# Performance work log

Measured on AMD Instinct MI355X. Metric: run time of the kernel, lower is better.

Reference implementation:

```python
import jax, jax.numpy as jnp
import numpy as np


def _ccl(x, w, b):
    # FFT-domain circular conv: rfft2 -> complex multiply + sum over c_in -> irfft2 + bias
    H, W = x.shape[-2], x.shape[-1]
    xf = jnp.fft.rfft2(x)                 # [B, Ci, H, Wf] complex
    wf = jnp.fft.rfft2(w, s=(H, W))       # [Co, Ci, H, Wf] complex
    hf = jnp.einsum('bihw,oihw->bohw', xf, wf)
    return jnp.fft.irfft2(hf, s=(H, W)) + b[:, None, None]


def _maxpool(x, ph, pw):
    B, C, H, W = x.shape
    return x.reshape(B, C, H // ph, ph, W // pw, pw).max(axis=(3, 5))


def _upsample_zero(x, sh, sw):
    B, C, H, W = x.shape
    y = jnp.zeros((B, C, H * sh, W * sw), dtype=x.dtype)
    return y.at[:, :, ::sh, ::sw].set(x)


def setup_inputs() -> dict:
    key = jax.random.key(0)
    ks = jax.random.split(key, 11)
    inp = {"x": jax.random.normal(ks[0], (16, 2, 64, 256), dtype=jnp.float32)}
    specs = [  # (c_out, c_in, kh, kw)
        (50, 1, 3, 7), (50, 50, 3, 7), (50, 50, 3, 5), (50, 50, 3, 7), (1, 50, 3, 7)]
    for i, (co, ci, kh, kw) in enumerate(specs):
        K = float(np.sqrt(1.0 / (ci * kh * kw)))
        inp[f"w{i+1}"] = (2 * jax.random.uniform(ks[2 * i + 1], (co, ci, kh, kw), dtype=jnp.float32) - 1) * K
        inp[f"b{i+1}"] = (2 * jax.random.uniform(ks[2 * i + 2], (co,), dtype=jnp.float32) - 1) * K
    return inp


def reference(x, w1, b1, w2, b2, w3, b3, w4, b4, w5, b5):
    H, W = x.shape[-2], x.shape[-1]
    h = x.reshape(-1, 1, H, W)                       # [2B, 1, 64, 256]
    h = jax.nn.relu(_maxpool(_ccl(h, w1, b1), 2, 4))  # [2B, 50, 32, 64]
    h = jax.nn.relu(_maxpool(_ccl(h, w2, b2), 2, 4))  # [2B, 50, 16, 16]
    h = h.reshape(-1, 2, h.shape[-3], h.shape[-2], h.shape[-1])
    h = h[:, 0] + h[:, 1].mean(axis=(-1, -2))[..., None, None]  # [B, 50, 16, 16]
    h = jax.nn.relu(_ccl(_upsample_zero(h, 2, 4), w3, b3))       # [B, 50, 32, 64]
    h = jax.nn.relu(_ccl(_upsample_zero(h, 2, 4), w4, b4))       # [B, 50, 64, 256]
    h = jax.nn.sigmoid(_ccl(h, w5, b5))                          # [B, 1, 64, 256]
    return h.squeeze(1)
```

## Files before the change

### kernel.cpp

```cpp
#include <hip/hip_runtime.h>
#include <math.h>

__global__ __launch_bounds__(256) void k1(const float* __restrict__ x,
                                          const float* __restrict__ w1,
                                          const float* __restrict__ b1,
                                          float* __restrict__ a1,
                                          const float* __restrict__ w2,
                                          const float* __restrict__ w3,
                                          const float* __restrict__ w4,
                                          float* __restrict__ w2t,
                                          float* __restrict__ w3t,
                                          float* __restrict__ w4t) {
  int b = blockIdx.z;
  int pr0 = blockIdx.x * 4;
  int co0 = blockIdx.y * 10;
  int ty = threadIdx.x >> 6;
  int pc = threadIdx.x & 63;
  int pr = pr0 + ty;
  const float* xb = x + b * (64 * 256);
  float xw[4][12];
#pragma unroll
  for (int r = 0; r < 4; ++r) {
    int row = (2 * pr - 2 + r) & 63;
    const float* rb = xb + row * 256;
#pragma unroll
    for (int v = 0; v < 3; ++v) {
      int col = (4 * pc - 8 + 4 * v) & 255;
      float4 t = *(const float4*)&rb[col];
      xw[r][4 * v + 0] = t.x; xw[r][4 * v + 1] = t.y;
      xw[r][4 * v + 2] = t.z; xw[r][4 * v + 3] = t.w;
    }
  }
#pragma unroll
  for (int cq = 0; cq < 10; ++cq) {
    int co = co0 + cq;
    const float* wp = w1 + co * 21;
    float m = -1e30f;
#pragma unroll
    for (int iy = 0; iy < 2; ++iy) {
#pragma unroll
      for (int jx = 0; jx < 4; ++jx) {
        float s = 0.f;
#pragma unroll
        for (int di = 0; di < 3; ++di)
#pragma unroll
          for (int dj = 0; dj < 7; ++dj)
            s = fmaf(xw[iy + 2 - di][jx + 8 - dj], wp[di * 7 + dj], s);
        m = fmaxf(m, s);
      }
    }
    float v = fmaxf(m + b1[co], 0.f);
    a1[((b * 50 + co) * 32 + pr) * 64 + pc] = v;
  }
  if (blockIdx.y == 0) {
    int base = (blockIdx.z * 8 + blockIdx.x) * 256 + threadIdx.x;
    for (int i = base; i < 90000; i += 65536) {
      if (i < 52500) {
        int co = i % 50, r = i / 50;
        w2t[i] = w2[co * 1050 + r];
        w4t[i] = w4[co * 1050 + r];
      } else {
        int j2 = i - 52500;
        int co = j2 % 50, r = j2 / 50;
        w3t[j2] = w3[co * 750 + r];
      }
    }
  }
}

__global__ __launch_bounds__(256) void k2(const float* __restrict__ a1,
                                          const float* __restrict__ w2t,
                                          const float* __restrict__ b2,
                                          float* __restrict__ a2) {
  __shared__ __align__(16) float sm[3840];
  int b = blockIdx.z;
  int r0 = blockIdx.x * 4;
  int co0 = blockIdx.y * 10;
  int y = threadIdx.x >> 6;
  int xcol = threadIdx.x & 63;
  const float* p[7];
#pragma unroll
  for (int dj = 0; dj < 7; ++dj) p[dj] = sm + y * 64 + ((xcol - dj) & 63);
  float acc[10];
#pragma unroll
  for (int co = 0; co < 10; ++co) acc[co] = b2[co0 + co];
  const float* ain = a1 + b * (50 * 2048);
  for (int cci = 0; cci < 5; ++cci) {
    __syncthreads();
    for (int e = threadIdx.x; e < 960; e += 256) {
      int ci = e / 96;
      int rem = e - ci * 96;
      int rr = rem >> 4;
      int c4 = rem & 15;
      int row = (r0 - 2 + rr) & 31;
      *(float4*)&sm[(ci * 6 + rr) * 64 + c4 * 4] =
          *(const float4*)&ain[(cci * 10 + ci) * 2048 + row * 64 + c4 * 4];
    }
    __syncthreads();
    const float* q0 = p[0]; const float* q1 = p[1]; const float* q2 = p[2];
    const float* q3 = p[3]; const float* q4 = p[4]; const float* q5 = p[5];
    const float* q6 = p[6];
    for (int ci = 0; ci < 10; ++ci) {
      const float* wci = w2t + (cci * 10 + ci) * 1050 + co0;
#pragma unroll
      for (int di = 0; di < 3; ++di) {
        const int ro = (2 - di) * 64;
        float xv0 = q0[ro], xv1 = q1[ro], xv2 = q2[ro], xv3 = q3[ro];
        float xv4 = q4[ro], xv5 = q5[ro], xv6 = q6[ro];
        const float* wr = wci + di * 7 * 50;
#pragma unroll
        for (int co = 0; co < 10; ++co) acc[co] = fmaf(xv0, wr[co], acc[co]);
#pragma unroll
        for (int co = 0; co < 10; ++co) acc[co] = fmaf(xv1, wr[50 + co], acc[co]);
#pragma unroll
        for (int co = 0; co < 10; ++co) acc[co] = fmaf(xv2, wr[100 + co], acc[co]);
#pragma unroll
        for (int co = 0; co < 10; ++co) acc[co] = fmaf(xv3, wr[150 + co], acc[co]);
#pragma unroll
        for (int co = 0; co < 10; ++co) acc[co] = fmaf(xv4, wr[200 + co], acc[co]);
#pragma unroll
        for (int co = 0; co < 10; ++co) acc[co] = fmaf(xv5, wr[250 + co], acc[co]);
#pragma unroll
        for (int co = 0; co < 10; ++co) acc[co] = fmaf(xv6, wr[300 + co], acc[co]);
      }
      q0 += 384; q1 += 384; q2 += 384; q3 += 384; q4 += 384; q5 += 384; q6 += 384;
    }
  }
  __syncthreads();
#pragma unroll
  for (int k = 0; k < 10; ++k)
    sm[k * 256 + y * 64 + xcol] = acc[k];
  __syncthreads();
  for (int w = threadIdx.x; w < 320; w += 256) {
    int cop = w / 32;
    int pr = (w >> 4) & 1;
    int pc = w & 15;
    float m = -1e30f;
#pragma unroll
    for (int yy = 0; yy < 2; ++yy)
#pragma unroll
      for (int xx = 0; xx < 4; ++xx)
        m = fmaxf(m, sm[cop * 256 + (pr * 2 + yy) * 64 + pc * 4 + xx]);
    m = fmaxf(m, 0.f);
    a2[((b * 50 + co0 + cop) * 16 + (r0 >> 1) + pr) * 16 + pc] = m;
  }
}

__global__ __launch_bounds__(512) void k3(const float* __restrict__ a2,
                                          const float* __restrict__ w3t,
                                          const float* __restrict__ b3,
                                          float* __restrict__ a3) {
  __shared__ float ts[4000];
  __shared__ float mean_s[64];
  __shared__ float part[200];
  int b = blockIdx.z;
  int r0 = blockIdx.x * 8;
  int co0 = blockIdx.y * 5;
  int tid = threadIdx.x;
  const float* aodd = a2 + (2 * b + 1) * (50 * 256);
  if (tid < 200) {
    int ci = tid >> 2, p = tid & 3;
    float s = 0.f;
    for (int k = 0; k < 64; ++k) s += aodd[ci * 256 + p * 64 + k];
    part[tid] = s;
  }
  __syncthreads();
  if (tid < 50)
    mean_s[tid] = (part[4 * tid] + part[4 * tid + 1] + part[4 * tid + 2] + part[4 * tid + 3]) * (1.f / 256.f);
  __syncthreads();
  const float* aev = a2 + (2 * b) * (50 * 256);
  for (int e = tid; e < 4000; e += 512) {
    int ci = e / 80;
    int rr = (e >> 4) % 5;
    int tc = e & 15;
    int trow = ((r0 >> 1) - 1 + rr) & 15;
    ts[e] = aev[ci * 256 + trow * 16 + tc] + mean_s[ci];
  }
  __syncthreads();
  int wv = __builtin_amdgcn_readfirstlane(tid >> 6);
  int lane = tid & 63;
  int p = wv >> 2;
  int m = wv & 3;
  int q = lane & 15;
  int yidx = lane >> 4;
  int i = r0 + 2 * yidx + p;
  int j = 4 * q + m;
  float acc[5];
#pragma unroll
  for (int co = 0; co < 5; ++co) acc[co] = b3[co0 + co];
  int ndi = (p == 0) ? 2 : 1;
  int ndj = (m == 0) ? 2 : 1;
  for (int aa = 0; aa < ndi; ++aa) {
    int di = (p == 0) ? (2 * aa) : 1;
    int rr = 1 + ((2 * yidx + p - di) >> 1);
    for (int e2 = 0; e2 < ndj; ++e2) {
      int dj = (m == 0) ? (4 * e2) : m;
      int tc = ((j - dj + 64) >> 2) & 15;
      for (int ci = 0; ci < 50; ++ci) {
        float xv = ts[ci * 80 + rr * 16 + tc];
        const float* wrow = w3t + (ci * 15 + di * 5 + dj) * 50 + co0;
#pragma unroll
        for (int co = 0; co < 5; ++co)
          acc[co] = fmaf(xv, wrow[co], acc[co]);
      }
    }
  }
  float* aout = a3 + b * (50 * 2048);
#pragma unroll
  for (int co = 0; co < 5; ++co)
    aout[(co0 + co) * 2048 + i * 64 + j] = fmaxf(acc[co], 0.f);
}

__global__ __launch_bounds__(512) void k4(const float* __restrict__ a3,
                                          const float* __restrict__ w4t,
                                          const float* __restrict__ b4,
                                          float* __restrict__ a4) {
  __shared__ __align__(16) float s4[9600];
  int b = blockIdx.z;
  int r0 = blockIdx.x * 4;
  int co0 = blockIdx.y * 10;
  int tid = threadIdx.x;
  const float* ain = a3 + b * (50 * 2048);
  int prb = (r0 >> 1) - 1;
  for (int e = tid; e < 2400; e += 512) {
    int ci = e / 48;
    int rem = e - ci * 48;
    int rr = rem >> 4;
    int c4 = rem & 15;
    int row = (prb + rr) & 31;
    *(float4*)&s4[(ci * 3 + rr) * 64 + c4 * 4] =
        *(const float4*)&ain[ci * 2048 + row * 64 + c4 * 4];
  }
  __syncthreads();
  int wv = __builtin_amdgcn_readfirstlane(tid >> 6);
  int lane = tid & 63;
  int rowsel = wv >> 2;
  int m = wv & 3;
  int j = 4 * lane + m;
  float acc[2][10];
#pragma unroll
  for (int co = 0; co < 10; ++co) {
    float bc = b4[co0 + co];
    acc[0][co] = bc; acc[1][co] = bc;
  }
  int ndi = (rowsel == 0) ? 2 : 1;
  int ndj = (m < 3) ? 2 : 1;
  for (int aa = 0; aa < ndi; ++aa) {
    int di = (rowsel == 0) ? (2 * aa) : 1;
    int rrb = 1 + ((rowsel - di) >> 1);
    for (int e2 = 0; e2 < ndj; ++e2) {
      int dj = m + 4 * e2;
      int tc = ((j - dj) >> 2) & 63;
      for (int ci = 0; ci < 50; ++ci) {
        float xv0 = s4[ci * 192 + rrb * 64 + tc];
        float xv1 = s4[ci * 192 + (rrb + 1) * 64 + tc];
        const float* wrow = w4t + (ci * 21 + di * 7 + dj) * 50 + co0;
#pragma unroll
        for (int co = 0; co < 10; ++co) {
          float w = wrow[co];
          acc[0][co] = fmaf(xv0, w, acc[0][co]);
          acc[1][co] = fmaf(xv1, w, acc[1][co]);
        }
      }
    }
  }
  float* aout = a4 + b * (50 * 16384);
  int i0 = r0 + rowsel, i1 = r0 + rowsel + 2;
#pragma unroll
  for (int co = 0; co < 10; ++co) {
    aout[(co0 + co) * 16384 + i0 * 256 + j] = fmaxf(acc[0][co], 0.f);
    aout[(co0 + co) * 16384 + i1 * 256 + j] = fmaxf(acc[1][co], 0.f);
  }
}

__global__ __launch_bounds__(512) void k5(const float* __restrict__ a4,
                                          const float* __restrict__ w5,
                                          const float* __restrict__ b5,
                                          float* __restrict__ out) {
  __shared__ __align__(16) float s5[4000];
  __shared__ float smw5[1056];
  int bid = blockIdx.x;
  int b = bid >> 5;
  int rem = bid & 31;
  int r0 = (rem >> 2) * 8;
  int jb = (rem & 3) * 64;
  int tid = threadIdx.x;
  int y = tid >> 6;
  int q = tid & 63;
  for (int e = tid; e < 1050; e += 512) smw5[e] = w5[e];
  float acc = b5[0];
  const float* ain = a4 + b * (50 * 16384);
  for (int cc = 0; cc < 10; ++cc) {
    __syncthreads();
    for (int e = tid; e < 1000; e += 512) {
      int ci = e / 200;
      int rem2 = e - ci * 200;
      int rr = rem2 / 20;
      int g = rem2 - rr * 20;
      int row = (r0 - 2 + rr) & 63;
      int col = (jb + 4 * g - 8) & 255;
      *(float4*)&s5[(ci * 10 + rr) * 80 + 4 * g] =
          *(const float4*)&ain[(cc * 5 + ci) * 16384 + row * 256 + col];
    }
    __syncthreads();
#pragma unroll
    for (int ci = 0; ci < 5; ++ci) {
#pragma unroll
      for (int di = 0; di < 3; ++di) {
        const float* base = s5 + ci * 800 + (y + 2 - di) * 80 + 8 + q;
        const float* wp = smw5 + ((cc * 5 + ci) * 3 + di) * 7;
#pragma unroll
        for (int dj = 0; dj < 7; ++dj)
          acc = fmaf(base[-dj], wp[dj], acc);
      }
    }
  }
  out[b * 16384 + (r0 + y) * 256 + jb + q] = 1.f / (1.f + expf(-acc));
}

extern "C" void kernel_launch(void* const* d_in, const int* in_sizes, int n_in,
                              void* d_out, int out_size, void* d_ws, size_t ws_size,
                              hipStream_t stream) {
  (void)in_sizes; (void)n_in; (void)out_size; (void)ws_size;
  const float* x  = (const float*)d_in[0];
  const float* w1 = (const float*)d_in[1];
  const float* b1 = (const float*)d_in[2];
  const float* w2 = (const float*)d_in[3];
  const float* b2 = (const float*)d_in[4];
  const float* w3 = (const float*)d_in[5];
  const float* b3 = (const float*)d_in[6];
  const float* w4 = (const float*)d_in[7];
  const float* b4 = (const float*)d_in[8];
  const float* w5 = (const float*)d_in[9];
  const float* b5 = (const float*)d_in[10];
  float* out = (float*)d_out;
  float* ws  = (float*)d_ws;
  float* w2t = ws;
  float* w3t = w2t + 52500;
  float* w4t = w3t + 37500;
  float* a1  = w4t + 52500;
  float* a2  = a1 + 32 * 50 * 32 * 64;
  float* a3  = a2 + 32 * 50 * 16 * 16;
  float* a4  = a3 + 16 * 50 * 32 * 64;
  hipLaunchKernelGGL(k1, dim3(8, 5, 32), dim3(256), 0, stream, x, w1, b1, a1,
                     w2, w3, w4, w2t, w3t, w4t);
  hipLaunchKernelGGL(k2, dim3(8, 5, 32), dim3(256), 0, stream, a1, w2t, b2, a2);
  hipLaunchKernelGGL(k3, dim3(4, 10, 16), dim3(512), 0, stream, a2, w3t, b3, a3);
  hipLaunchKernelGGL(k4, dim3(16, 5, 16), dim3(512), 0, stream, a3, w4t, b4, a4);
  hipLaunchKernelGGL(k5, dim3(512), dim3(512), 0, stream, a4, w5, b5, out);
}
```

Measured before the change: 306.5 us.

## Replace shared-memory input staging in k2 with register prefetch and wave shuffles

The second conv kernel no longer stages input tiles into LDS behind barriers. Each thread loads its three input rows per channel straight from global memory into registers, prefetching the next channel, and gets the horizontally shifted taps with 64-wide wave shuffles. This removes the block-wide syncs and LDS traffic in the main loop. In exchange it issues six cross-lane shuffles per row and does uncoalesced-free but unshared global loads, which may cost about the same as the LDS reads.

```diff
diff --git a/kernel.cpp b/kernel.cpp
--- a/kernel.cpp
+++ b/kernel.cpp
@@ -72,64 +72,57 @@
                                           const float* __restrict__ w2t,
                                           const float* __restrict__ b2,
                                           float* __restrict__ a2) {
-  __shared__ __align__(16) float sm[3840];
+  __shared__ float sm[2560];
   int b = blockIdx.z;
   int r0 = blockIdx.x * 4;
   int co0 = blockIdx.y * 10;
   int y = threadIdx.x >> 6;
-  int xcol = threadIdx.x & 63;
-  const float* p[7];
-#pragma unroll
-  for (int dj = 0; dj < 7; ++dj) p[dj] = sm + y * 64 + ((xcol - dj) & 63);
+  int lane = threadIdx.x & 63;
+  int offA = ((r0 + y - 2) & 31) * 64 + lane;
+  int offB = ((r0 + y - 1) & 31) * 64 + lane;
+  int offC = ((r0 + y) & 31) * 64 + lane;
+  int idx1 = (lane - 1) & 63, idx2 = (lane - 2) & 63, idx3 = (lane - 3) & 63;
+  int idx4 = (lane - 4) & 63, idx5 = (lane - 5) & 63, idx6 = (lane - 6) & 63;
   float acc[10];
 #pragma unroll
   for (int co = 0; co < 10; ++co) acc[co] = b2[co0 + co];
   const float* ain = a1 + b * (50 * 2048);
-  for (int cci = 0; cci < 5; ++cci) {
-    __syncthreads();
-    for (int e = threadIdx.x; e < 960; e += 256) {
-      int ci = e / 96;
-      int rem = e - ci * 96;
-      int rr = rem >> 4;
-      int c4 = rem & 15;
-      int row = (r0 - 2 + rr) & 31;
-      *(float4*)&sm[(ci * 6 + rr) * 64 + c4 * 4] =
-          *(const float4*)&ain[(cci * 10 + ci) * 2048 + row * 64 + c4 * 4];
-    }
-    __syncthreads();
-    const float* q0 = p[0]; const float* q1 = p[1]; const float* q2 = p[2];
-    const float* q3 = p[3]; const float* q4 = p[4]; const float* q5 = p[5];
-    const float* q6 = p[6];
-    for (int ci = 0; ci < 10; ++ci) {
-      const float* wci = w2t + (cci * 10 + ci) * 1050 + co0;
-#pragma unroll
-      for (int di = 0; di < 3; ++di) {
-        const int ro = (2 - di) * 64;
-        float xv0 = q0[ro], xv1 = q1[ro], xv2 = q2[ro], xv3 = q3[ro];
-        float xv4 = q4[ro], xv5 = q5[ro], xv6 = q6[ro];
-        const float* wr = wci + di * 7 * 50;
-#pragma unroll
-        for (int co = 0; co < 10; ++co) acc[co] = fmaf(xv0, wr[co], acc[co]);
-#pragma unroll
-        for (int co = 0; co < 10; ++co) acc[co] = fmaf(xv1, wr[50 + co], acc[co]);
-#pragma unroll
-        for (int co = 0; co < 10; ++co) acc[co] = fmaf(xv2, wr[100 + co], acc[co]);
-#pragma unroll
-        for (int co = 0; co < 10; ++co) acc[co] = fmaf(xv3, wr[150 + co], acc[co]);
-#pragma unroll
-        for (int co = 0; co < 10; ++co) acc[co] = fmaf(xv4, wr[200 + co], acc[co]);
-#pragma unroll
-        for (int co = 0; co < 10; ++co) acc[co] = fmaf(xv5, wr[250 + co], acc[co]);
-#pragma unroll
-        for (int co = 0; co < 10; ++co) acc[co] = fmaf(xv6, wr[300 + co], acc[co]);
-      }
-      q0 += 384; q1 += 384; q2 += 384; q3 += 384; q4 += 384; q5 += 384; q6 += 384;
-    }
-  }
-  __syncthreads();
+  float vA = ain[offA], vB = ain[offB], vC = ain[offC];
+  for (int ci = 0; ci < 50; ++ci) {
+    int cin = (ci + 1 < 50) ? (ci + 1) : 49;
+    const float* np = ain + cin * 2048;
+    float nA = np[offA], nB = np[offB], nC = np[offC];
+    const float* wci = w2t + ci * 1050 + co0;
+#pragma unroll
+    for (int di = 0; di < 3; ++di) {
+      float v = (di == 0) ? vC : (di == 1) ? vB : vA;
+      const float* wr = wci + di * 350;
+      float x1 = __shfl(v, idx1, 64);
+      float x2 = __shfl(v, idx2, 64);
+      float x3 = __shfl(v, idx3, 64);
+      float x4 = __shfl(v, idx4, 64);
+      float x5 = __shfl(v, idx5, 64);
+      float x6 = __shfl(v, idx6, 64);
+#pragma unroll
+      for (int co = 0; co < 10; ++co) acc[co] = fmaf(v,  wr[co], acc[co]);
+#pragma unroll
+      for (int co = 0; co < 10; ++co) acc[co] = fmaf(x1, wr[50 + co], acc[co]);
+#pragma unroll
+      for (int co = 0; co < 10; ++co) acc[co] = fmaf(x2, wr[100 + co], acc[co]);
+#pragma unroll
+      for (int co = 0; co < 10; ++co) acc[co] = fmaf(x3, wr[150 + co], acc[co]);
+#pragma unroll
+      for (int co = 0; co < 10; ++co) acc[co] = fmaf(x4, wr[200 + co], acc[co]);
+#pragma unroll
+      for (int co = 0; co < 10; ++co) acc[co] = fmaf(x5, wr[250 + co], acc[co]);
+#pragma unroll
+      for (int co = 0; co < 10; ++co) acc[co] = fmaf(x6, wr[300 + co], acc[co]);
+    }
+    vA = nA; vB = nB; vC = nC;
+  }
 #pragma unroll
   for (int k = 0; k < 10; ++k)
-    sm[k * 256 + y * 64 + xcol] = acc[k];
+    sm[k * 256 + y * 64 + lane] = acc[k];
   __syncthreads();
   for (int w = threadIdx.x; w < 320; w += 256) {
     int cop = w / 32;
```

New measurement: 302.2 us. No clear change (-1.4%).
